# Performance work log

Measured on AMD Instinct MI355X. Metric: run time of the kernel, lower is better.

Reference implementation:

```python
import jax, jax.numpy as jnp
import numpy as np

M, K, O = 8192, 4096, 4096
WORDS = K // 32
INT32_MAX = 2147483647


def _unpack_ternary(nz, sgn):
    """Unpack bit-packed ternary weights.
    nz, sgn: [O, WORDS] int32 bitmasks. Bit j of word w corresponds to input
    column w*32 + j. weight = 0 if nz bit clear, else +1 (sgn bit clear) or -1.
    Returns dense float32 [O, K].
    """
    shifts = jnp.arange(32, dtype=jnp.uint32)
    nzb = (nz.astype(jnp.uint32)[:, :, None] >> shifts) & jnp.uint32(1)   # [O, WORDS, 32]
    sgb = (sgn.astype(jnp.uint32)[:, :, None] >> shifts) & jnp.uint32(1)  # [O, WORDS, 32]
    w = nzb.astype(jnp.float32) * (1.0 - 2.0 * sgb.astype(jnp.float32))
    return w.reshape(nz.shape[0], -1)  # [O, K]


def setup_inputs() -> dict:
    key = jax.random.key(0)
    k1, k2, k3, k4, k5 = jax.random.split(key, 5)
    x = jax.random.normal(k1, (M, K), dtype=jnp.float32)
    nz = jax.random.randint(k2, (O, WORDS), 0, INT32_MAX, dtype=jnp.int32)
    sgn = jax.random.randint(k3, (O, WORDS), 0, INT32_MAX, dtype=jnp.int32)
    bias = jax.random.normal(k4, (O,), dtype=jnp.float32) * 0.01
    alpha = jax.random.uniform(k5, (O,), dtype=jnp.float32, minval=0.5, maxval=1.5)
    return {"x": x, "nz": nz, "sgn": sgn, "bias": bias, "alpha": alpha}


def reference(x, nz, sgn, bias, alpha):
    # y = (x @ W^T) * alpha + bias, W dequantized from ternary bit-packs
    W = _unpack_ternary(nz, sgn)                       # [O, K]
    y = jnp.einsum('mk,ok->mo', x, W)                  # [M, O]
    y = y * alpha[None, :] + bias[None, :]
    return y
```

## Files before the change

kernel.cpp:

```cpp
#include <hip/hip_runtime.h>
#include <stdint.h>

#define M_DIM 8192
#define K_DIM 4096
#define O_DIM 4096
#define NWORDS 128

#define BM 128
#define BN 128
#define BK 32

typedef __attribute__((ext_vector_type(8))) short bf16x8;
typedef __attribute__((ext_vector_type(4))) float f32x4;

__device__ __forceinline__ unsigned f32_to_bf16u(float f) {
  union { float f; unsigned u; } v; v.f = f;
  return (v.u + 0x7FFFu + ((v.u >> 16) & 1u)) >> 16;
}

__device__ __forceinline__ unsigned pack_bf16x2(float lo, float hi) {
  return f32_to_bf16u(lo) | (f32_to_bf16u(hi) << 16);
}

__global__ __launch_bounds__(256) void cvt_x_kernel(const float* __restrict__ x,
                                                    unsigned short* __restrict__ xb) {
  long i = ((long)blockIdx.x * 256 + threadIdx.x) * 8;
  const float4 a = *(const float4*)(x + i);
  const float4 b = *(const float4*)(x + i + 4);
  uint4 o;
  o.x = pack_bf16x2(a.x, a.y);
  o.y = pack_bf16x2(a.z, a.w);
  o.z = pack_bf16x2(b.x, b.y);
  o.w = pack_bf16x2(b.z, b.w);
  *(uint4*)(xb + i) = o;
}

__global__ __launch_bounds__(256) void unpack_w_kernel(const unsigned* __restrict__ nz,
                                                       const unsigned* __restrict__ sgn,
                                                       unsigned short* __restrict__ wb) {
  const int idx = blockIdx.x * 256 + threadIdx.x;
  const unsigned n = nz[idx];
  const unsigned s = sgn[idx];
  unsigned out[16];
#pragma unroll
  for (int p = 0; p < 16; ++p) {
    const int j0 = 2 * p, j1 = 2 * p + 1;
    unsigned lo = ((n >> j0) & 1u) ? (0x3F80u | (((s >> j0) & 1u) << 15)) : 0u;
    unsigned hi = ((n >> j1) & 1u) ? (0x3F80u | (((s >> j1) & 1u) << 15)) : 0u;
    out[p] = lo | (hi << 16);
  }
  uint4* dst = (uint4*)(wb + (long)idx * 32);
#pragma unroll
  for (int q = 0; q < 4; ++q)
    dst[q] = make_uint4(out[4 * q], out[4 * q + 1], out[4 * q + 2], out[4 * q + 3]);
}

__global__ __launch_bounds__(256) void gemm_kernel(const unsigned short* __restrict__ A,
                                                   const unsigned short* __restrict__ B,
                                                   const float* __restrict__ bias,
                                                   const float* __restrict__ alpha,
                                                   float* __restrict__ C) {
  __shared__ unsigned short lA[BM * BK];
  __shared__ unsigned short lB[BN * BK];

  const int tid  = threadIdx.x;
  const int lane = tid & 63;
  const int wave = tid >> 6;
  const int mBlk = blockIdx.y * BM;
  const int nBlk = blockIdx.x * BN;

  const int o0 = tid * 16;
  const int o1 = o0 + 4096;
  const int r0 = o0 >> 6, c0 = (o0 & 63) >> 1;
  const int r1 = o1 >> 6, c1 = (o1 & 63) >> 1;

  const unsigned short* gA0 = A + (long)(mBlk + r0) * K_DIM + c0;
  const unsigned short* gA1 = A + (long)(mBlk + r1) * K_DIM + c1;
  const unsigned short* gB0 = B + (long)(nBlk + r0) * K_DIM + c0;
  const unsigned short* gB1 = B + (long)(nBlk + r1) * K_DIM + c1;

  char* lAc = (char*)lA;
  char* lBc = (char*)lB;

  const int wm = (wave >> 1) * 64;
  const int wn = (wave & 1) * 64;
  const int fr = lane & 15;
  const int fq = lane >> 4;

  f32x4 acc[4][4] = {};

  for (int kt = 0; kt < K_DIM; kt += BK) {
    __builtin_amdgcn_global_load_lds((const __attribute__((address_space(1))) void*)(gA0 + kt),
                                     (__attribute__((address_space(3))) void*)(lAc + o0), 16, 0, 0);
    __builtin_amdgcn_global_load_lds((const __attribute__((address_space(1))) void*)(gA1 + kt),
                                     (__attribute__((address_space(3))) void*)(lAc + o1), 16, 0, 0);
    __builtin_amdgcn_global_load_lds((const __attribute__((address_space(1))) void*)(gB0 + kt),
                                     (__attribute__((address_space(3))) void*)(lBc + o0), 16, 0, 0);
    __builtin_amdgcn_global_load_lds((const __attribute__((address_space(1))) void*)(gB1 + kt),
                                     (__attribute__((address_space(3))) void*)(lBc + o1), 16, 0, 0);
    __syncthreads();

    bf16x8 af[4], bfv[4];
#pragma unroll
    for (int t = 0; t < 4; ++t) {
      af[t]  = *(const bf16x8*)(lA + (wm + t * 16 + fr) * BK + fq * 8);
      bfv[t] = *(const bf16x8*)(lB + (wn + t * 16 + fr) * BK + fq * 8);
    }
#pragma unroll
    for (int tm = 0; tm < 4; ++tm)
#pragma unroll
      for (int tn = 0; tn < 4; ++tn)
        acc[tm][tn] = __builtin_amdgcn_mfma_f32_16x16x32_bf16(af[tm], bfv[tn], acc[tm][tn], 0, 0, 0);
    __syncthreads();
  }

#pragma unroll
  for (int tn = 0; tn < 4; ++tn) {
    const int n = nBlk + wn + tn * 16 + fr;
    const float al = alpha[n];
    const float bi = bias[n];
#pragma unroll
    for (int tm = 0; tm < 4; ++tm) {
      const int mBase = mBlk + wm + tm * 16 + fq * 4;
#pragma unroll
      for (int r = 0; r < 4; ++r)
        C[(long)(mBase + r) * O_DIM + n] = acc[tm][tn][r] * al + bi;
    }
  }
}

__global__ __launch_bounds__(256) void fallback_kernel(const float* __restrict__ x,
                                                       const unsigned* __restrict__ nz,
                                                       const unsigned* __restrict__ sgn,
                                                       const float* __restrict__ bias,
                                                       const float* __restrict__ alpha,
                                                       float* __restrict__ y) {
  long gid = (long)blockIdx.x * 256 + threadIdx.x;
  int o = (int)(gid % O_DIM);
  long m = gid / O_DIM;
  const float* xr = x + m * K_DIM;
  float s = 0.f;
  for (int w = 0; w < NWORDS; ++w) {
    unsigned n = nz[o * NWORDS + w];
    unsigned g = sgn[o * NWORDS + w];
    for (int j = 0; j < 32; ++j) {
      if ((n >> j) & 1u) {
        float v = xr[w * 32 + j];
        s += ((g >> j) & 1u) ? -v : v;
      }
    }
  }
  y[gid] = s * alpha[o] + bias[o];
}

extern "C" void kernel_launch(void* const* d_in, const int* in_sizes, int n_in,
                              void* d_out, int out_size, void* d_ws, size_t ws_size,
                              hipStream_t stream) {
  const float*    x     = (const float*)d_in[0];
  const unsigned* nz    = (const unsigned*)d_in[1];
  const unsigned* sgn   = (const unsigned*)d_in[2];
  const float*    bias  = (const float*)d_in[3];
  const float*    alpha = (const float*)d_in[4];
  float*          y     = (float*)d_out;

  const size_t xb_bytes = (size_t)M_DIM * K_DIM * 2;
  const size_t wb_bytes = (size_t)O_DIM * K_DIM * 2;

  if (ws_size >= xb_bytes + wb_bytes) {
    unsigned short* xb = (unsigned short*)d_ws;
    unsigned short* wb = (unsigned short*)((char*)d_ws + xb_bytes);

    cvt_x_kernel<<<(M_DIM * (long)K_DIM) / (8 * 256), 256, 0, stream>>>(x, xb);
    unpack_w_kernel<<<(O_DIM * NWORDS) / 256, 256, 0, stream>>>(nz, sgn, wb);
    dim3 grid(O_DIM / BN, M_DIM / BM);
    gemm_kernel<<<grid, 256, 0, stream>>>(xb, wb, bias, alpha, y);
  } else {
    fallback_kernel<<<(long)M_DIM * O_DIM / 256, 256, 0, stream>>>(x, nz, sgn, bias, alpha, y);
  }
}
```

Measured before the change: 522.6 us.

## Double GEMM K-tile with XOR-swizzled LDS layout and nontemporal streaming

Raises the GEMM K-tile from 32 to 64 so each barrier pair covers two MFMA k-steps, which halves the number of synchronizations. The LDS layout gets an XOR swizzle on 16-byte chunks to avoid bank conflicts on fragment reads. The x conversion kernel now handles 16 floats per thread using nontemporal loads, and the output stores are nontemporal. The trade-off is double the LDS per block, which may lower occupancy, and the nontemporal hints could hurt cache behaviour.

Measured after the change: 498.4 us. 4.6% less time.

```diff
diff --git a/kernel.cpp b/kernel.cpp
--- a/kernel.cpp
+++ b/kernel.cpp
@@ -8,10 +8,12 @@
 
 #define BM 128
 #define BN 128
-#define BK 32
+#define BK 64
 
 typedef __attribute__((ext_vector_type(8))) short bf16x8;
 typedef __attribute__((ext_vector_type(4))) float f32x4;
+typedef __attribute__((ext_vector_type(4))) float fvec4;
+typedef __attribute__((ext_vector_type(4))) unsigned uvec4;
 
 __device__ __forceinline__ unsigned f32_to_bf16u(float f) {
   union { float f; unsigned u; } v; v.f = f;
@@ -22,17 +24,20 @@
   return f32_to_bf16u(lo) | (f32_to_bf16u(hi) << 16);
 }
 
-__global__ __launch_bounds__(256) void cvt_x_kernel(const float* __restrict__ x,
-                                                    unsigned short* __restrict__ xb) {
-  long i = ((long)blockIdx.x * 256 + threadIdx.x) * 8;
-  const float4 a = *(const float4*)(x + i);
-  const float4 b = *(const float4*)(x + i + 4);
-  uint4 o;
-  o.x = pack_bf16x2(a.x, a.y);
-  o.y = pack_bf16x2(a.z, a.w);
-  o.z = pack_bf16x2(b.x, b.y);
-  o.w = pack_bf16x2(b.z, b.w);
-  *(uint4*)(xb + i) = o;
+__global__ __launch_bounds__(256) void cvt_x_kernel(const fvec4* __restrict__ x,
+                                                    uvec4* __restrict__ xb) {
+  const long t = (long)blockIdx.x * 256 + threadIdx.x;
+  const fvec4 a = __builtin_nontemporal_load(x + 4 * t + 0);
+  const fvec4 b = __builtin_nontemporal_load(x + 4 * t + 1);
+  const fvec4 c = __builtin_nontemporal_load(x + 4 * t + 2);
+  const fvec4 d = __builtin_nontemporal_load(x + 4 * t + 3);
+  uvec4 o0, o1;
+  o0.x = pack_bf16x2(a.x, a.y);  o0.y = pack_bf16x2(a.z, a.w);
+  o0.z = pack_bf16x2(b.x, b.y);  o0.w = pack_bf16x2(b.z, b.w);
+  o1.x = pack_bf16x2(c.x, c.y);  o1.y = pack_bf16x2(c.z, c.w);
+  o1.z = pack_bf16x2(d.x, d.y);  o1.w = pack_bf16x2(d.z, d.w);
+  xb[2 * t] = o0;
+  xb[2 * t + 1] = o1;
 }
 
 __global__ __launch_bounds__(256) void unpack_w_kernel(const unsigned* __restrict__ nz,
@@ -49,10 +54,12 @@
     unsigned hi = ((n >> j1) & 1u) ? (0x3F80u | (((s >> j1) & 1u) << 15)) : 0u;
     out[p] = lo | (hi << 16);
   }
-  uint4* dst = (uint4*)(wb + (long)idx * 32);
+  uvec4* dst = (uvec4*)(wb + (long)idx * 32);
 #pragma unroll
-  for (int q = 0; q < 4; ++q)
-    dst[q] = make_uint4(out[4 * q], out[4 * q + 1], out[4 * q + 2], out[4 * q + 3]);
+  for (int q = 0; q < 4; ++q) {
+    uvec4 v = { out[4 * q], out[4 * q + 1], out[4 * q + 2], out[4 * q + 3] };
+    dst[q] = v;
+  }
 }
 
 __global__ __launch_bounds__(256) void gemm_kernel(const unsigned short* __restrict__ A,
@@ -69,16 +76,18 @@
   const int mBlk = blockIdx.y * BM;
   const int nBlk = blockIdx.x * BN;
 
-  const int o0 = tid * 16;
-  const int o1 = o0 + 4096;
-  const int r0 = o0 >> 6, c0 = (o0 & 63) >> 1;
-  const int r1 = o1 >> 6, c1 = (o1 & 63) >> 1;
-
-  const unsigned short* gA0 = A + (long)(mBlk + r0) * K_DIM + c0;
-  const unsigned short* gA1 = A + (long)(mBlk + r1) * K_DIM + c1;
-  const unsigned short* gB0 = B + (long)(nBlk + r0) * K_DIM + c0;
-  const unsigned short* gB1 = B + (long)(nBlk + r1) * K_DIM + c1;
-
+  int oArr[4];
+  const unsigned short *gA[4], *gB[4];
+#pragma unroll
+  for (int j = 0; j < 4; ++j) {
+    const int oj = tid * 16 + j * 4096;
+    const int r  = oj >> 7;
+    const int qp = (oj >> 4) & 7;
+    const int q  = qp ^ (r & 7);
+    gA[j] = A + (long)(mBlk + r) * K_DIM + q * 8;
+    gB[j] = B + (long)(nBlk + r) * K_DIM + q * 8;
+    oArr[j] = oj;
+  }
   char* lAc = (char*)lA;
   char* lBc = (char*)lB;
 
@@ -90,27 +99,33 @@
   f32x4 acc[4][4] = {};
 
   for (int kt = 0; kt < K_DIM; kt += BK) {
-    __builtin_amdgcn_global_load_lds((const __attribute__((address_space(1))) void*)(gA0 + kt),
-                                     (__attribute__((address_space(3))) void*)(lAc + o0), 16, 0, 0);
-    __builtin_amdgcn_global_load_lds((const __attribute__((address_space(1))) void*)(gA1 + kt),
-                                     (__attribute__((address_space(3))) void*)(lAc + o1), 16, 0, 0);
-    __builtin_amdgcn_global_load_lds((const __attribute__((address_space(1))) void*)(gB0 + kt),
-                                     (__attribute__((address_space(3))) void*)(lBc + o0), 16, 0, 0);
-    __builtin_amdgcn_global_load_lds((const __attribute__((address_space(1))) void*)(gB1 + kt),
-                                     (__attribute__((address_space(3))) void*)(lBc + o1), 16, 0, 0);
+#pragma unroll
+    for (int j = 0; j < 4; ++j) {
+      __builtin_amdgcn_global_load_lds((const __attribute__((address_space(1))) void*)(gA[j] + kt),
+                                       (__attribute__((address_space(3))) void*)(lAc + oArr[j]), 16, 0, 0);
+      __builtin_amdgcn_global_load_lds((const __attribute__((address_space(1))) void*)(gB[j] + kt),
+                                       (__attribute__((address_space(3))) void*)(lBc + oArr[j]), 16, 0, 0);
+    }
     __syncthreads();
 
-    bf16x8 af[4], bfv[4];
 #pragma unroll
-    for (int t = 0; t < 4; ++t) {
-      af[t]  = *(const bf16x8*)(lA + (wm + t * 16 + fr) * BK + fq * 8);
-      bfv[t] = *(const bf16x8*)(lB + (wn + t * 16 + fr) * BK + fq * 8);
+    for (int kh = 0; kh < 2; ++kh) {
+      bf16x8 af[4], bfv[4];
+#pragma unroll
+      for (int t = 0; t < 4; ++t) {
+        const int rA = wm + t * 16 + fr;
+        const int qA = (kh * 4 + fq) ^ (rA & 7);
+        af[t] = *(const bf16x8*)(lA + rA * BK + qA * 8);
+        const int rB = wn + t * 16 + fr;
+        const int qB = (kh * 4 + fq) ^ (rB & 7);
+        bfv[t] = *(const bf16x8*)(lB + rB * BK + qB * 8);
+      }
+#pragma unroll
+      for (int tm = 0; tm < 4; ++tm)
+#pragma unroll
+        for (int tn = 0; tn < 4; ++tn)
+          acc[tm][tn] = __builtin_amdgcn_mfma_f32_16x16x32_bf16(af[tm], bfv[tn], acc[tm][tn], 0, 0, 0);
     }
-#pragma unroll
-    for (int tm = 0; tm < 4; ++tm)
-#pragma unroll
-      for (int tn = 0; tn < 4; ++tn)
-        acc[tm][tn] = __builtin_amdgcn_mfma_f32_16x16x32_bf16(af[tm], bfv[tn], acc[tm][tn], 0, 0, 0);
     __syncthreads();
   }
 
@@ -124,7 +139,8 @@
       const int mBase = mBlk + wm + tm * 16 + fq * 4;
 #pragma unroll
       for (int r = 0; r < 4; ++r)
-        C[(long)(mBase + r) * O_DIM + n] = acc[tm][tn][r] * al + bi;
+        __builtin_nontemporal_store(acc[tm][tn][r] * al + bi,
+                                    C + (long)(mBase + r) * O_DIM + n);
     }
   }
 }
@@ -170,7 +186,7 @@
     unsigned short* xb = (unsigned short*)d_ws;
     unsigned short* wb = (unsigned short*)((char*)d_ws + xb_bytes);
 
-    cvt_x_kernel<<<(M_DIM * (long)K_DIM) / (8 * 256), 256, 0, stream>>>(x, xb);
+    cvt_x_kernel<<<(M_DIM * (long)K_DIM) / (16 * 256), 256, 0, stream>>>((const fvec4*)x, (uvec4*)xb);
     unpack_w_kernel<<<(O_DIM * NWORDS) / 256, 256, 0, stream>>>(nz, sgn, wb);
     dim3 grid(O_DIM / BN, M_DIM / BM);
     gemm_kernel<<<grid, 256, 0, stream>>>(xb, wb, bias, alpha, y);
```
